# Optimization experiments

Hardware: AMD Instinct MI355X
Metric: run time of the kernel (lower is better)

Reference implementation:

```python
import jax, jax.numpy as jnp
import numpy as np

NB = 64        # number of chains = batch.max()+1 (static for reshape)
NPER = 131072  # points per chain
NTYPES = 16
NITER = 10
ACC = 1e-9


def setup_inputs() -> dict:
    key = jax.random.key(0)
    k1, k2, k3 = jax.random.split(key, 3)
    x = jax.random.normal(k1, (NB * NPER, 3), dtype=jnp.float32)
    d0 = jax.random.uniform(k2, (NTYPES, NTYPES), dtype=jnp.float32, minval=0.5, maxval=1.5)
    z = jax.random.randint(k3, (NB * NPER,), 0, NTYPES)
    batch = jnp.repeat(jnp.arange(NB), NPER)  # contiguous chain ids
    return {"x": x, "d0": d0, "batch": batch, "z": z}


def _diffT(C):
    # adjoint of the forward difference stencil: [nb, n-1, 3] -> [nb, n, 3]
    mid = C[:, :-1] - C[:, 1:]
    return jnp.concatenate([-C[:, :1], mid, C[:, -1:]], axis=1)


def _constraint(r, d):
    # r: [nb, n, 3], d: [nb, n-1, 1]; c_i = |r_{i+1}-r_i|^2 - d_i^2
    dx = r[:, 1:] - r[:, :-1]
    c = jnp.sum(dx * dx, axis=-1, keepdims=True) - d * d
    return c, dx


def _line_search(x_sg, lam_sg, d_sg, alpha0, cnorm):
    # emulates the torch.no_grad() backtracking line search
    def eval_ctry(a):
        rt = (x_sg - a * lam_sg).reshape(NB, NPER, 3)
        ct, _ = _constraint(rt, d_sg)
        return jnp.sum(ct * ct)

    def cond(s):
        return ~s[3]

    def body(s):
        alpha, lsiter, _, _ = s
        ctry = eval_ctry(alpha)
        ok = ctry < cnorm
        new_alpha = jnp.where(ok, alpha, alpha * 0.5)
        new_lsiter = jnp.where(ok, lsiter, lsiter + 1)
        done = ok | (new_lsiter > 10)
        return (new_alpha, new_lsiter, ctry, done)

    init = (alpha0, jnp.int32(0), jnp.float32(jnp.inf), jnp.bool_(False))
    alpha, lsiter, ctry, _ = jax.lax.while_loop(cond, body, init)
    # if no backtracking happened and not converged, grow the step
    alpha = jnp.where((lsiter == 0) & (ctry > ACC), alpha * 1.5, alpha)
    return alpha, ctry


def _forward(x, d0, z):
    z2 = z.reshape(NB, NPER)
    # gather-based distance lookup for consecutive pairs: [NB, NPER-1, 1]
    d = d0[z2[:, :-1], z2[:, 1:]].astype(x.dtype)[..., None]
    d_sg = jax.lax.stop_gradient(d)
    x_cur = x
    alpha = jnp.float32(0.0)
    done = jnp.bool_(False)
    for j in range(NITER):
        r = x_cur.reshape(NB, NPER, 3)
        c, dx = _constraint(r, d)               # [NB, NPER-1, 1], [NB, NPER-1, 3]
        lam = 2.0 * _diffT(c * dx)              # dConstraintT2: [NB, NPER, 3]
        lam_x = lam.reshape(-1, 3)
        cnorm = jnp.sum(c * c)
        x_sg = jax.lax.stop_gradient(x_cur)
        lam_sg = jax.lax.stop_gradient(lam_x)
        cnorm_sg = jax.lax.stop_gradient(cnorm)
        alpha0 = (1.0 / jnp.linalg.norm(lam_sg)) if j == 0 else alpha
        alpha_j, ctry = _line_search(x_sg, lam_sg, d_sg, alpha0, cnorm_sg)
        x_new = x_cur - alpha_j * lam_x
        # freeze updates after convergence (emulates the torch early break)
        x_cur = jnp.where(done, x_cur, x_new)
        alpha = jnp.where(done, alpha, alpha_j)
        done = done | (ctry < ACC)
    return x_cur


def reference(x, d0, batch, z):
    # batch only encodes nb = batch.max()+1; layout is contiguous chains (static NB)
    return _forward(x, d0, z)
```

## Files before the change

kernel.cpp:

```cpp
#include <hip/hip_runtime.h>

#define NB 64
#define NPER 131072
#define NTYPES 16
#define NITER 10
#define ACCV 1e-9

#define TB 256
#define TILES_PER_CHAIN (NPER / TB)
#define TILES_TOTAL (NB * TILES_PER_CHAIN)
#define RED_BLOCKS 4096

struct LSState {
  double alpha;
  double alpha_step;
  int done;
  int do_update;
};

__device__ inline double wave_sum64(double v) {
  #pragma unroll
  for (int o = 32; o > 0; o >>= 1) v += __shfl_down(v, o, 64);
  return v;
}

__global__ void pc_init(LSState* st) {
  st->alpha = 0.0;
  st->alpha_step = 0.0;
  st->done = 0;
  st->do_update = 1;
}

__global__ __launch_bounds__(TB) void pc_reduce(const float* __restrict__ x,
    const int* __restrict__ z, const float* __restrict__ d0,
    double* __restrict__ partials) {
  __shared__ float xs[(TB + 3) * 3];
  __shared__ int zs[TB + 3];
  __shared__ float d0s[NTYPES * NTYPES];
  __shared__ double redl[5][TB / 64];
  const int tid = threadIdx.x;
  if (tid < NTYPES * NTYPES) d0s[tid] = d0[tid];
  double s0 = 0, s1 = 0, s2 = 0, s3 = 0, s4 = 0;
  for (int tile = blockIdx.x; tile < TILES_TOTAL; tile += RED_BLOCKS) {
    const int b = tile / TILES_PER_CHAIN;
    const int s = (tile % TILES_PER_CHAIN) * TB;
    const int base = b * NPER;
    __syncthreads();
    const int gf0 = (base + s - 1) * 3;
    const int lo = base * 3, hi = (base + NPER) * 3;
    for (int f = tid; f < (TB + 3) * 3; f += TB) {
      const int g = gf0 + f;
      xs[f] = (g >= lo && g < hi) ? x[g] : 0.f;
    }
    for (int idx = tid; idx < TB + 3; idx += TB) {
      const int p = s - 1 + idx;
      zs[idx] = (p >= 0 && p < NPER) ? z[base + p] : 0;
    }
    __syncthreads();
    const int i = s + tid;
    if (i <= NPER - 2) {
      float C[3][3];
      float dxc[3] = {0.f, 0.f, 0.f};
      float cc = 0.f;
      #pragma unroll
      for (int k = 0; k < 3; ++k) {
        const int j = i - 1 + k;
        if (j >= 0 && j <= NPER - 2) {
          const int lp = j - (s - 1);
          const int l = lp * 3;
          const float dxv = xs[l + 3] - xs[l + 0];
          const float dyv = xs[l + 4] - xs[l + 1];
          const float dzv = xs[l + 5] - xs[l + 2];
          const float dd = d0s[zs[lp] * NTYPES + zs[lp + 1]];
          const float c = dxv * dxv + dyv * dyv + dzv * dzv - dd * dd;
          C[k][0] = c * dxv; C[k][1] = c * dyv; C[k][2] = c * dzv;
          if (k == 1) { dxc[0] = dxv; dxc[1] = dyv; dxc[2] = dzv; cc = c; }
        } else {
          C[k][0] = 0.f; C[k][1] = 0.f; C[k][2] = 0.f;
        }
      }
      const float gx = 2.f * (2.f * C[1][0] - C[0][0] - C[2][0]);
      const float gy = 2.f * (2.f * C[1][1] - C[0][1] - C[2][1]);
      const float gz = 2.f * (2.f * C[1][2] - C[0][2] - C[2][2]);
      const float A = gx * gx + gy * gy + gz * gz;
      const float Bv = -2.f * (dxc[0] * gx + dxc[1] * gy + dxc[2] * gz);
      s0 += (double)cc * (double)cc;
      s1 += 2.0 * (double)cc * (double)Bv;
      s2 += (double)Bv * (double)Bv + 2.0 * (double)cc * (double)A;
      s3 += 2.0 * (double)A * (double)Bv;
      s4 += (double)A * (double)A;
    }
  }
  const int wave = tid >> 6, lane = tid & 63;
  double v[5] = {s0, s1, s2, s3, s4};
  #pragma unroll
  for (int k = 0; k < 5; ++k) {
    const double w = wave_sum64(v[k]);
    if (lane == 0) redl[k][wave] = w;
  }
  __syncthreads();
  if (tid == 0) {
    #pragma unroll
    for (int k = 0; k < 5; ++k)
      partials[k * RED_BLOCKS + blockIdx.x] =
          redl[k][0] + redl[k][1] + redl[k][2] + redl[k][3];
  }
}

__global__ __launch_bounds__(256) void pc_linesearch(
    const double* __restrict__ partials, LSState* st, int iter) {
  __shared__ double redl[5][4];
  const int tid = threadIdx.x;
  double v[5] = {0, 0, 0, 0, 0};
  for (int i = tid; i < RED_BLOCKS; i += 256) {
    #pragma unroll
    for (int k = 0; k < 5; ++k) v[k] += partials[k * RED_BLOCKS + i];
  }
  const int wave = tid >> 6, lane = tid & 63;
  #pragma unroll
  for (int k = 0; k < 5; ++k) {
    const double w = wave_sum64(v[k]);
    if (lane == 0) redl[k][wave] = w;
  }
  __syncthreads();
  if (tid == 0) {
    double S[5];
    #pragma unroll
    for (int k = 0; k < 5; ++k)
      S[k] = redl[k][0] + redl[k][1] + redl[k][2] + redl[k][3];
    const double cnorm = S[0];
    double alpha = (iter == 0) ? 1.0 / sqrt(-0.5 * S[1]) : st->alpha;
    int lsiter = 0;
    double ctry;
    for (;;) {
      ctry = S[0] + alpha * (S[1] + alpha * (S[2] + alpha * (S[3] + alpha * S[4])));
      if (ctry < cnorm) break;
      alpha *= 0.5;
      if (++lsiter > 10) break;
    }
    if (lsiter == 0 && ctry > ACCV) alpha *= 1.5;
    const int done_prev = st->done;
    st->alpha_step = alpha;
    st->do_update = done_prev ? 0 : 1;
    if (!done_prev) st->alpha = alpha;
    st->done = done_prev | ((ctry < ACCV) ? 1 : 0);
  }
}

__global__ __launch_bounds__(TB) void pc_update(float* __restrict__ x,
    const int* __restrict__ z, const float* __restrict__ d0,
    const LSState* __restrict__ st) {
  if (!st->do_update) return;
  __shared__ float xs[(TB + 2) * 3];
  __shared__ int zs[TB + 2];
  __shared__ float d0s[NTYPES * NTYPES];
  const int tid = threadIdx.x;
  const int tile = blockIdx.x;
  const int b = tile / TILES_PER_CHAIN;
  const int s = (tile % TILES_PER_CHAIN) * TB;
  const int base = b * NPER;
  if (tid < NTYPES * NTYPES) d0s[tid] = d0[tid];
  const int gf0 = (base + s - 1) * 3;
  const int lo = base * 3, hi = (base + NPER) * 3;
  for (int f = tid; f < (TB + 2) * 3; f += TB) {
    const int g = gf0 + f;
    xs[f] = (g >= lo && g < hi) ? x[g] : 0.f;
  }
  for (int idx = tid; idx < TB + 2; idx += TB) {
    const int p = s - 1 + idx;
    zs[idx] = (p >= 0 && p < NPER) ? z[base + p] : 0;
  }
  __syncthreads();
  const int p = s + tid;
  const float alpha = (float)st->alpha_step;
  float Cm[3], Cc[3];
  #pragma unroll
  for (int k = 0; k < 2; ++k) {
    const int j = p - 1 + k;
    float* Co = (k == 0) ? Cm : Cc;
    if (j >= 0 && j <= NPER - 2) {
      const int lp = j - (s - 1);
      const int l = lp * 3;
      const float dxv = xs[l + 3] - xs[l + 0];
      const float dyv = xs[l + 4] - xs[l + 1];
      const float dzv = xs[l + 5] - xs[l + 2];
      const float dd = d0s[zs[lp] * NTYPES + zs[lp + 1]];
      const float c = dxv * dxv + dyv * dyv + dzv * dzv - dd * dd;
      Co[0] = c * dxv; Co[1] = c * dyv; Co[2] = c * dzv;
    } else {
      Co[0] = 0.f; Co[1] = 0.f; Co[2] = 0.f;
    }
  }
  const float lx = 2.f * (Cm[0] - Cc[0]);
  const float ly = 2.f * (Cm[1] - Cc[1]);
  const float lz = 2.f * (Cm[2] - Cc[2]);
  const int li = (tid + 1) * 3;
  const int g = (base + p) * 3;
  x[g + 0] = xs[li + 0] - alpha * lx;
  x[g + 1] = xs[li + 1] - alpha * ly;
  x[g + 2] = xs[li + 2] - alpha * lz;
}

extern "C" void kernel_launch(void* const* d_in, const int* in_sizes, int n_in,
                              void* d_out, int out_size, void* d_ws, size_t ws_size,
                              hipStream_t stream) {
  const float* d0 = (const float*)d_in[1];
  const int* z = (const int*)d_in[3];
  float* x = (float*)d_out;
  LSState* st = (LSState*)d_ws;
  double* partials = (double*)((char*)d_ws + 256);

  hipMemcpyAsync(d_out, d_in[0], (size_t)NB * NPER * 3 * sizeof(float),
                 hipMemcpyDeviceToDevice, stream);
  pc_init<<<1, 1, 0, stream>>>(st);
  for (int j = 0; j < NITER; ++j) {
    pc_reduce<<<RED_BLOCKS, TB, 0, stream>>>(x, z, d0, partials);
    pc_linesearch<<<1, 256, 0, stream>>>(partials, st, j);
    pc_update<<<TILES_TOTAL, TB, 0, stream>>>(x, z, d0, st);
  }
}
```

Measured before the change: 1.445 ms.

## Fuse update with next reduction and fold line search via last-block ticket

```diff
diff --git a/kernel.cpp b/kernel.cpp
--- a/kernel.cpp
+++ b/kernel.cpp
@@ -9,13 +9,15 @@
 #define TB 256
 #define TILES_PER_CHAIN (NPER / TB)
 #define TILES_TOTAL (NB * TILES_PER_CHAIN)
-#define RED_BLOCKS 4096
-
-struct LSState {
+#define FBLOCKS 2048
+#define TPB (TILES_TOTAL / FBLOCKS)
+
+struct PCState {
   double alpha;
   double alpha_step;
   int done;
   int do_update;
+  unsigned ticket;
 };
 
 __device__ inline double wave_sum64(double v) {
@@ -24,181 +26,194 @@
   return v;
 }
 
-__global__ void pc_init(LSState* st) {
+__global__ void pc_init(PCState* st) {
   st->alpha = 0.0;
   st->alpha_step = 0.0;
   st->done = 0;
   st->do_update = 1;
-}
-
-__global__ __launch_bounds__(TB) void pc_reduce(const float* __restrict__ x,
+  st->ticket = 0u;
+}
+
+template <int MODE>
+__global__ __launch_bounds__(TB) void pc_fused(
+    const float* __restrict__ xin, float* __restrict__ xout,
     const int* __restrict__ z, const float* __restrict__ d0,
-    double* __restrict__ partials) {
-  __shared__ float xs[(TB + 3) * 3];
-  __shared__ int zs[TB + 3];
+    PCState* st, double* __restrict__ part, int iter) {
+  __shared__ float xs[(TB + 5) * 3];
+  __shared__ float xn[(TB + 3) * 3];
+  __shared__ float Cold[(TB + 4) * 3];
+  __shared__ float ds2[TB + 4];
+  __shared__ float Cnew[(TB + 2) * 3];
+  __shared__ float cnw[TB + 2];
+  __shared__ float dxn[(TB + 2) * 3];
+  __shared__ int zs[TB + 5];
   __shared__ float d0s[NTYPES * NTYPES];
   __shared__ double redl[5][TB / 64];
+  __shared__ int islast;
+
   const int tid = threadIdx.x;
-  if (tid < NTYPES * NTYPES) d0s[tid] = d0[tid];
+  d0s[tid] = d0[tid];
+  const float alpha = (MODE == 0 || !st->do_update) ? 0.f : (float)st->alpha_step;
   double s0 = 0, s1 = 0, s2 = 0, s3 = 0, s4 = 0;
-  for (int tile = blockIdx.x; tile < TILES_TOTAL; tile += RED_BLOCKS) {
+
+  for (int tt = 0; tt < TPB; ++tt) {
+    const int tile = blockIdx.x * TPB + tt;
     const int b = tile / TILES_PER_CHAIN;
-    const int s = (tile % TILES_PER_CHAIN) * TB;
+    const int t = tile % TILES_PER_CHAIN;
+    const int P0 = t * TB;
     const int base = b * NPER;
     __syncthreads();
-    const int gf0 = (base + s - 1) * 3;
-    const int lo = base * 3, hi = (base + NPER) * 3;
-    for (int f = tid; f < (TB + 3) * 3; f += TB) {
-      const int g = gf0 + f;
-      xs[f] = (g >= lo && g < hi) ? x[g] : 0.f;
-    }
-    for (int idx = tid; idx < TB + 3; idx += TB) {
-      const int p = s - 1 + idx;
-      zs[idx] = (p >= 0 && p < NPER) ? z[base + p] : 0;
-    }
-    __syncthreads();
-    const int i = s + tid;
-    if (i <= NPER - 2) {
-      float C[3][3];
-      float dxc[3] = {0.f, 0.f, 0.f};
-      float cc = 0.f;
+
+    {
+      const int gf0 = (base + P0 - 2) * 3;
+      const int lo = base * 3, hi = (base + NPER) * 3;
+      for (int f = tid; f < (TB + 5) * 3; f += TB) {
+        const int g = gf0 + f;
+        xs[f] = (g >= lo && g < hi) ? xin[g] : 0.f;
+      }
+      for (int q = tid; q < TB + 5; q += TB) {
+        const int p = P0 - 2 + q;
+        zs[q] = (p >= 0 && p < NPER) ? z[base + p] : 0;
+      }
+    }
+    __syncthreads();
+
+    for (int q = tid; q < TB + 4; q += TB) {
+      const int j = P0 - 2 + q;
+      float cx = 0.f, cy = 0.f, cz = 0.f, dd2 = 0.f;
+      if (j >= 0 && j <= NPER - 2) {
+        const int l = q * 3;
+        const float ax = xs[l + 3] - xs[l + 0];
+        const float ay = xs[l + 4] - xs[l + 1];
+        const float az = xs[l + 5] - xs[l + 2];
+        const float dd = d0s[zs[q] * NTYPES + zs[q + 1]];
+        dd2 = dd * dd;
+        const float c = ax * ax + ay * ay + az * az - dd2;
+        cx = c * ax; cy = c * ay; cz = c * az;
+      }
+      Cold[q * 3 + 0] = cx; Cold[q * 3 + 1] = cy; Cold[q * 3 + 2] = cz;
+      ds2[q] = dd2;
+    }
+    __syncthreads();
+
+    for (int q = tid; q < TB + 3; q += TB) {
+      const int p = P0 - 1 + q;
+      float nx = 0.f, ny = 0.f, nz = 0.f;
+      if (p >= 0 && p < NPER) {
+        const int l = (q + 1) * 3;
+        const int cb = q * 3;
+        const float lx = 2.f * (Cold[cb + 0] - Cold[cb + 3]);
+        const float ly = 2.f * (Cold[cb + 1] - Cold[cb + 4]);
+        const float lz = 2.f * (Cold[cb + 2] - Cold[cb + 5]);
+        nx = xs[l + 0] - alpha * lx;
+        ny = xs[l + 1] - alpha * ly;
+        nz = xs[l + 2] - alpha * lz;
+        if (MODE != 0 && p >= P0 && p < P0 + TB) {
+          const int g = (base + p) * 3;
+          xout[g + 0] = nx; xout[g + 1] = ny; xout[g + 2] = nz;
+        }
+      }
+      xn[q * 3 + 0] = nx; xn[q * 3 + 1] = ny; xn[q * 3 + 2] = nz;
+    }
+
+    if (MODE != 2) {
+      __syncthreads();
+      for (int q = tid; q < TB + 2; q += TB) {
+        const int j = P0 - 1 + q;
+        float c = 0.f, ax = 0.f, ay = 0.f, az = 0.f;
+        if (j >= 0 && j <= NPER - 2) {
+          const int l = q * 3;
+          ax = xn[l + 3] - xn[l + 0];
+          ay = xn[l + 4] - xn[l + 1];
+          az = xn[l + 5] - xn[l + 2];
+          c = ax * ax + ay * ay + az * az - ds2[q + 1];
+        }
+        cnw[q] = c;
+        dxn[q * 3 + 0] = ax; dxn[q * 3 + 1] = ay; dxn[q * 3 + 2] = az;
+        Cnew[q * 3 + 0] = c * ax; Cnew[q * 3 + 1] = c * ay; Cnew[q * 3 + 2] = c * az;
+      }
+      __syncthreads();
+
+      const int i = P0 + tid;
+      if (i <= NPER - 2) {
+        const int l = (tid + 1) * 3;
+        const float gx = 2.f * (2.f * Cnew[l + 0] - Cnew[l - 3] - Cnew[l + 3]);
+        const float gy = 2.f * (2.f * Cnew[l + 1] - Cnew[l - 2] - Cnew[l + 4]);
+        const float gz = 2.f * (2.f * Cnew[l + 2] - Cnew[l - 1] - Cnew[l + 5]);
+        const float A = gx * gx + gy * gy + gz * gz;
+        const float Bv = -2.f * (dxn[l + 0] * gx + dxn[l + 1] * gy + dxn[l + 2] * gz);
+        const float c = cnw[tid + 1];
+        s0 += (double)c * (double)c;
+        s1 += 2.0 * (double)c * (double)Bv;
+        s2 += (double)Bv * (double)Bv + 2.0 * (double)c * (double)A;
+        s3 += 2.0 * (double)A * (double)Bv;
+        s4 += (double)A * (double)A;
+      }
+    }
+  }
+
+  if (MODE == 2) return;
+
+  {
+    double v[5] = {s0, s1, s2, s3, s4};
+    const int wave = tid >> 6, lane = tid & 63;
+    #pragma unroll
+    for (int k = 0; k < 5; ++k) {
+      const double w = wave_sum64(v[k]);
+      if (lane == 0) redl[k][wave] = w;
+    }
+    __syncthreads();
+    if (tid == 0) {
       #pragma unroll
-      for (int k = 0; k < 3; ++k) {
-        const int j = i - 1 + k;
-        if (j >= 0 && j <= NPER - 2) {
-          const int lp = j - (s - 1);
-          const int l = lp * 3;
-          const float dxv = xs[l + 3] - xs[l + 0];
-          const float dyv = xs[l + 4] - xs[l + 1];
-          const float dzv = xs[l + 5] - xs[l + 2];
-          const float dd = d0s[zs[lp] * NTYPES + zs[lp + 1]];
-          const float c = dxv * dxv + dyv * dyv + dzv * dzv - dd * dd;
-          C[k][0] = c * dxv; C[k][1] = c * dyv; C[k][2] = c * dzv;
-          if (k == 1) { dxc[0] = dxv; dxc[1] = dyv; dxc[2] = dzv; cc = c; }
-        } else {
-          C[k][0] = 0.f; C[k][1] = 0.f; C[k][2] = 0.f;
-        }
-      }
-      const float gx = 2.f * (2.f * C[1][0] - C[0][0] - C[2][0]);
-      const float gy = 2.f * (2.f * C[1][1] - C[0][1] - C[2][1]);
-      const float gz = 2.f * (2.f * C[1][2] - C[0][2] - C[2][2]);
-      const float A = gx * gx + gy * gy + gz * gz;
-      const float Bv = -2.f * (dxc[0] * gx + dxc[1] * gy + dxc[2] * gz);
-      s0 += (double)cc * (double)cc;
-      s1 += 2.0 * (double)cc * (double)Bv;
-      s2 += (double)Bv * (double)Bv + 2.0 * (double)cc * (double)A;
-      s3 += 2.0 * (double)A * (double)Bv;
-      s4 += (double)A * (double)A;
-    }
-  }
-  const int wave = tid >> 6, lane = tid & 63;
-  double v[5] = {s0, s1, s2, s3, s4};
-  #pragma unroll
-  for (int k = 0; k < 5; ++k) {
-    const double w = wave_sum64(v[k]);
-    if (lane == 0) redl[k][wave] = w;
-  }
-  __syncthreads();
-  if (tid == 0) {
+      for (int k = 0; k < 5; ++k)
+        part[k * FBLOCKS + blockIdx.x] =
+            redl[k][0] + redl[k][1] + redl[k][2] + redl[k][3];
+      __threadfence();
+      const unsigned tk = atomicAdd(&st->ticket, 1u);
+      islast = (tk == FBLOCKS - 1) ? 1 : 0;
+    }
+    __syncthreads();
+    if (!islast) return;
+  }
+
+  __threadfence();
+  {
+    double v[5] = {0, 0, 0, 0, 0};
+    for (int i = tid; i < FBLOCKS; i += TB) {
+      #pragma unroll
+      for (int k = 0; k < 5; ++k) v[k] += part[k * FBLOCKS + i];
+    }
+    const int wave = tid >> 6, lane = tid & 63;
     #pragma unroll
-    for (int k = 0; k < 5; ++k)
-      partials[k * RED_BLOCKS + blockIdx.x] =
-          redl[k][0] + redl[k][1] + redl[k][2] + redl[k][3];
-  }
-}
-
-__global__ __launch_bounds__(256) void pc_linesearch(
-    const double* __restrict__ partials, LSState* st, int iter) {
-  __shared__ double redl[5][4];
-  const int tid = threadIdx.x;
-  double v[5] = {0, 0, 0, 0, 0};
-  for (int i = tid; i < RED_BLOCKS; i += 256) {
-    #pragma unroll
-    for (int k = 0; k < 5; ++k) v[k] += partials[k * RED_BLOCKS + i];
-  }
-  const int wave = tid >> 6, lane = tid & 63;
-  #pragma unroll
-  for (int k = 0; k < 5; ++k) {
-    const double w = wave_sum64(v[k]);
-    if (lane == 0) redl[k][wave] = w;
-  }
-  __syncthreads();
-  if (tid == 0) {
-    double S[5];
-    #pragma unroll
-    for (int k = 0; k < 5; ++k)
-      S[k] = redl[k][0] + redl[k][1] + redl[k][2] + redl[k][3];
-    const double cnorm = S[0];
-    double alpha = (iter == 0) ? 1.0 / sqrt(-0.5 * S[1]) : st->alpha;
-    int lsiter = 0;
-    double ctry;
-    for (;;) {
-      ctry = S[0] + alpha * (S[1] + alpha * (S[2] + alpha * (S[3] + alpha * S[4])));
-      if (ctry < cnorm) break;
-      alpha *= 0.5;
-      if (++lsiter > 10) break;
-    }
-    if (lsiter == 0 && ctry > ACCV) alpha *= 1.5;
-    const int done_prev = st->done;
-    st->alpha_step = alpha;
-    st->do_update = done_prev ? 0 : 1;
-    if (!done_prev) st->alpha = alpha;
-    st->done = done_prev | ((ctry < ACCV) ? 1 : 0);
-  }
-}
-
-__global__ __launch_bounds__(TB) void pc_update(float* __restrict__ x,
-    const int* __restrict__ z, const float* __restrict__ d0,
-    const LSState* __restrict__ st) {
-  if (!st->do_update) return;
-  __shared__ float xs[(TB + 2) * 3];
-  __shared__ int zs[TB + 2];
-  __shared__ float d0s[NTYPES * NTYPES];
-  const int tid = threadIdx.x;
-  const int tile = blockIdx.x;
-  const int b = tile / TILES_PER_CHAIN;
-  const int s = (tile % TILES_PER_CHAIN) * TB;
-  const int base = b * NPER;
-  if (tid < NTYPES * NTYPES) d0s[tid] = d0[tid];
-  const int gf0 = (base + s - 1) * 3;
-  const int lo = base * 3, hi = (base + NPER) * 3;
-  for (int f = tid; f < (TB + 2) * 3; f += TB) {
-    const int g = gf0 + f;
-    xs[f] = (g >= lo && g < hi) ? x[g] : 0.f;
-  }
-  for (int idx = tid; idx < TB + 2; idx += TB) {
-    const int p = s - 1 + idx;
-    zs[idx] = (p >= 0 && p < NPER) ? z[base + p] : 0;
-  }
-  __syncthreads();
-  const int p = s + tid;
-  const float alpha = (float)st->alpha_step;
-  float Cm[3], Cc[3];
-  #pragma unroll
-  for (int k = 0; k < 2; ++k) {
-    const int j = p - 1 + k;
-    float* Co = (k == 0) ? Cm : Cc;
-    if (j >= 0 && j <= NPER - 2) {
-      const int lp = j - (s - 1);
-      const int l = lp * 3;
-      const float dxv = xs[l + 3] - xs[l + 0];
-      const float dyv = xs[l + 4] - xs[l + 1];
-      const float dzv = xs[l + 5] - xs[l + 2];
-      const float dd = d0s[zs[lp] * NTYPES + zs[lp + 1]];
-      const float c = dxv * dxv + dyv * dyv + dzv * dzv - dd * dd;
-      Co[0] = c * dxv; Co[1] = c * dyv; Co[2] = c * dzv;
-    } else {
-      Co[0] = 0.f; Co[1] = 0.f; Co[2] = 0.f;
-    }
-  }
-  const float lx = 2.f * (Cm[0] - Cc[0]);
-  const float ly = 2.f * (Cm[1] - Cc[1]);
-  const float lz = 2.f * (Cm[2] - Cc[2]);
-  const int li = (tid + 1) * 3;
-  const int g = (base + p) * 3;
-  x[g + 0] = xs[li + 0] - alpha * lx;
-  x[g + 1] = xs[li + 1] - alpha * ly;
-  x[g + 2] = xs[li + 2] - alpha * lz;
+    for (int k = 0; k < 5; ++k) {
+      const double w = wave_sum64(v[k]);
+      if (lane == 0) redl[k][wave] = w;
+    }
+    __syncthreads();
+    if (tid == 0) {
+      double S[5];
+      #pragma unroll
+      for (int k = 0; k < 5; ++k)
+        S[k] = redl[k][0] + redl[k][1] + redl[k][2] + redl[k][3];
+      const double cnorm = S[0];
+      double alpha2 = (iter == 0) ? 1.0 / sqrt(-0.5 * S[1]) : st->alpha;
+      int lsiter = 0;
+      double ctry;
+      for (;;) {
+        ctry = S[0] + alpha2 * (S[1] + alpha2 * (S[2] + alpha2 * (S[3] + alpha2 * S[4])));
+        if (ctry < cnorm) break;
+        alpha2 *= 0.5;
+        if (++lsiter > 10) break;
+      }
+      if (lsiter == 0 && ctry > ACCV) alpha2 *= 1.5;
+      const int done_prev = st->done;
+      st->alpha_step = alpha2;
+      st->do_update = done_prev ? 0 : 1;
+      if (!done_prev) st->alpha = alpha2;
+      st->done = done_prev | ((ctry < ACCV) ? 1 : 0);
+      st->ticket = 0u;
+    }
+  }
 }
 
 extern "C" void kernel_launch(void* const* d_in, const int* in_sizes, int n_in,
@@ -206,16 +221,20 @@
                               hipStream_t stream) {
   const float* d0 = (const float*)d_in[1];
   const int* z = (const int*)d_in[3];
-  float* x = (float*)d_out;
-  LSState* st = (LSState*)d_ws;
-  double* partials = (double*)((char*)d_ws + 256);
-
-  hipMemcpyAsync(d_out, d_in[0], (size_t)NB * NPER * 3 * sizeof(float),
-                 hipMemcpyDeviceToDevice, stream);
+  float* ping = (float*)d_in[0];
+  float* dout = (float*)d_out;
+  PCState* st = (PCState*)d_ws;
+  double* part = (double*)((char*)d_ws + 256);
+  const size_t xbytes = (size_t)NB * NPER * 3 * sizeof(float);
+
+  hipMemcpyAsync(dout, ping, xbytes, hipMemcpyDeviceToDevice, stream);
   pc_init<<<1, 1, 0, stream>>>(st);
-  for (int j = 0; j < NITER; ++j) {
-    pc_reduce<<<RED_BLOCKS, TB, 0, stream>>>(x, z, d0, partials);
-    pc_linesearch<<<1, 256, 0, stream>>>(partials, st, j);
-    pc_update<<<TILES_TOTAL, TB, 0, stream>>>(x, z, d0, st);
-  }
-}
+  pc_fused<0><<<FBLOCKS, TB, 0, stream>>>(dout, dout, z, d0, st, part, 0);
+  float* a = dout;
+  float* bufb = ping;
+  for (int j = 1; j <= 9; ++j) {
+    pc_fused<1><<<FBLOCKS, TB, 0, stream>>>(a, bufb, z, d0, st, part, j);
+    float* tmp = a; a = bufb; bufb = tmp;
+  }
+  pc_fused<2><<<FBLOCKS, TB, 0, stream>>>(a, bufb, z, d0, st, part, 10);
+}
```

Measured after the change: 1.527 ms. +5.7%, slower.
